# Kernel tuning notes

Hardware: AMD Instinct MI355X
Metric: run time of the kernel (lower is better)

The kernel has to match this reference:

```python
import jax, jax.numpy as jnp
import numpy as np

NEG_SLOPE = 0.2


def gat_layer(h, src, dst, W, al, ar, b, num_nodes):
    # h: [N, Din], W: [Din, H*F], al/ar: [H, F], b: [H*F]
    H, F = al.shape
    feat = (h @ W).reshape(-1, H, F)                      # [N, H, F]
    el = jnp.sum(feat * al[None], axis=-1)                # [N, H]
    er = jnp.sum(feat * ar[None], axis=-1)                # [N, H]
    e = el[src] + er[dst]                                 # [E, H]
    e = jnp.where(e > 0, e, NEG_SLOPE * e)                # leaky_relu(0.2)
    # edge softmax over incoming edges of each dst node (per head)
    m = jax.ops.segment_max(e, dst, num_segments=num_nodes)   # [N, H]
    m = jnp.where(jnp.isfinite(m), m, 0.0)
    a = jnp.exp(e - m[dst])                               # [E, H]
    s = jax.ops.segment_sum(a, dst, num_segments=num_nodes)   # [N, H]
    alpha = a / jnp.maximum(s[dst], 1e-9)                 # [E, H]
    msg = feat[src] * alpha[:, :, None]                   # [E, H, F]
    out = jax.ops.segment_sum(msg, dst, num_segments=num_nodes)  # [N, H, F]
    out = out + b.reshape(H, F)[None]
    return out.reshape(-1, H * F)                         # view(-1, H*F)


def setup_inputs() -> dict:
    key = jax.random.key(0)
    ks = jax.random.split(key, 16)
    N, E, Din, Hh, F = 50000, 800000, 256, 4, 64
    s = 0.05
    return {
        "h": jax.random.normal(ks[0], (N, Din), jnp.float32),
        "src": jax.random.randint(ks[1], (E,), 0, N),
        "dst": jax.random.randint(ks[2], (E,), 0, N),
        "dst_node_ids": jax.random.randint(ks[3], (1024,), 0, N),
        "W0": jax.random.normal(ks[4], (Din, Hh * F), jnp.float32) * s,
        "al0": jax.random.normal(ks[5], (Hh, F), jnp.float32) * s,
        "ar0": jax.random.normal(ks[6], (Hh, F), jnp.float32) * s,
        "b0": jnp.zeros((Hh * F,), jnp.float32),
        "W1": jax.random.normal(ks[7], (Hh * F, Hh * F), jnp.float32) * s,
        "al1": jax.random.normal(ks[8], (Hh, F), jnp.float32) * s,
        "ar1": jax.random.normal(ks[9], (Hh, F), jnp.float32) * s,
        "b1": jnp.zeros((Hh * F,), jnp.float32),
        "W2": jax.random.normal(ks[10], (Hh * F, F), jnp.float32) * s,
        "al2": jax.random.normal(ks[11], (1, F), jnp.float32) * s,
        "ar2": jax.random.normal(ks[12], (1, F), jnp.float32) * s,
        "b2": jnp.zeros((F,), jnp.float32),
    }


def reference(h, src, dst, dst_node_ids,
              W0, al0, ar0, b0, W1, al1, ar1, b1, W2, al2, ar2, b2):
    N = h.shape[0]
    h = h.astype(jnp.float32)
    h = gat_layer(h, src, dst, W0, al0, ar0, b0, N)
    h = gat_layer(h, src, dst, W1, al1, ar1, b1, N)
    h = gat_layer(h, src, dst, W2, al2, ar2, b2, N)
    return h, dst_node_ids
```

## Files before the change

kernel.cpp:

```cpp
#include <hip/hip_runtime.h>
#include <hip/hip_bf16.h>

#define NEG_SLOPE 0.2f

typedef __attribute__((ext_vector_type(8))) short bf16x8;
typedef __attribute__((ext_vector_type(4))) float f32x4;

static inline int cdiv(int a, int b) { return (a + b - 1) / b; }

__device__ inline unsigned short f2bf(float x) {
  __hip_bfloat16 b = __float2bfloat16(x);
  return *reinterpret_cast<unsigned short*>(&b);
}
__device__ inline float bf2f(unsigned short u) {
  unsigned int v = (unsigned int)u << 16;
  return *reinterpret_cast<float*>(&v);
}

__global__ void splitT_all(const float* __restrict__ W0, unsigned short* __restrict__ W0hi,
                           unsigned short* __restrict__ W0lo,
                           const float* __restrict__ W1, unsigned short* __restrict__ W1hi,
                           unsigned short* __restrict__ W1lo,
                           const float* __restrict__ W2, unsigned short* __restrict__ W2hi,
                           unsigned short* __restrict__ W2lo) {
  const int S0 = 256 * 256, S1 = 256 * 256, S2 = 256 * 64;
  int i = blockIdx.x * blockDim.x + threadIdx.x;
  const float* W; unsigned short *hi, *lo; int K, Mo, perm;
  if (i < S0) { W = W0; hi = W0hi; lo = W0lo; K = 256; Mo = 256; perm = 0; }
  else if (i < S0 + S1) { i -= S0; W = W1; hi = W1hi; lo = W1lo; K = 256; Mo = 256; perm = 1; }
  else if (i < S0 + S1 + S2) { i -= S0 + S1; W = W2; hi = W2hi; lo = W2lo; K = 256; Mo = 64; perm = 1; }
  else return;
  int k = i / Mo, m = i - k * Mo;
  int kk = perm ? ((k & 63) * 4 + (k >> 6)) : k;
  float v = W[i];
  unsigned short h = f2bf(v);
  hi[(size_t)m * K + kk] = h;
  lo[(size_t)m * K + kk] = f2bf(v - bf2f(h));
}

template <int NF, bool CVT>
__global__ __launch_bounds__(256) void gemm_split(
    const unsigned short* __restrict__ Ahi, const float* __restrict__ Af32,
    const unsigned short* __restrict__ BThi, const unsigned short* __restrict__ BTlo,
    unsigned short* __restrict__ Chi,
    const float* __restrict__ alv, const float* __restrict__ arv,
    float* __restrict__ el, float* __restrict__ er, int Hn, int M, int K, int Ncols) {
  constexpr int BN = NF * 32;
  __shared__ unsigned short As[128][40];
  __shared__ unsigned short Bs[BN][88];
  const int tid = threadIdx.x;
  const int row0 = blockIdx.x * 128;
  const int col0 = blockIdx.y * BN;
  const int wid = tid >> 6, lane = tid & 63;
  const int wm = wid >> 1, wn = wid & 1;
  const int l15 = lane & 15, lg = lane >> 4;
  f32x4 acc[4][NF];
#pragma unroll
  for (int m = 0; m < 4; ++m)
#pragma unroll
    for (int n = 0; n < NF; ++n) acc[m][n] = (f32x4){0.f, 0.f, 0.f, 0.f};

  const uint4 zero4 = {0u, 0u, 0u, 0u};
  for (int k0 = 0; k0 < K; k0 += 32) {
    {
      int r = tid >> 2;
      const int kg = tid & 3;
#pragma unroll
      for (int it = 0; it < 2; ++it, r += 64) {
        const int grow = row0 + r;
        if constexpr (CVT) {
          float4 f0 = make_float4(0.f, 0.f, 0.f, 0.f), f1 = f0;
          if (grow < M) {
            f0 = *reinterpret_cast<const float4*>(&Af32[(size_t)grow * K + k0 + kg * 8]);
            f1 = *reinterpret_cast<const float4*>(&Af32[(size_t)grow * K + k0 + kg * 8 + 4]);
          }
          unsigned short t[8];
          t[0] = f2bf(f0.x); t[1] = f2bf(f0.y); t[2] = f2bf(f0.z); t[3] = f2bf(f0.w);
          t[4] = f2bf(f1.x); t[5] = f2bf(f1.y); t[6] = f2bf(f1.z); t[7] = f2bf(f1.w);
          *reinterpret_cast<uint4*>(&As[r][kg * 8]) = *reinterpret_cast<const uint4*>(t);
        } else {
          uint4 vh = zero4;
          if (grow < M) vh = *reinterpret_cast<const uint4*>(&Ahi[(size_t)grow * K + k0 + kg * 8]);
          *reinterpret_cast<uint4*>(&As[r][kg * 8]) = vh;
        }
      }
    }
    {
      int r = tid >> 2;
      const int kg = tid & 3;
#pragma unroll
      for (int it = 0; it < BN / 64; ++it, r += 64) {
        const int gcol = col0 + r;
        uint4 vh = *reinterpret_cast<const uint4*>(&BThi[(size_t)gcol * K + k0 + kg * 8]);
        uint4 vl = *reinterpret_cast<const uint4*>(&BTlo[(size_t)gcol * K + k0 + kg * 8]);
        *reinterpret_cast<uint4*>(&Bs[r][kg * 8]) = vh;
        *reinterpret_cast<uint4*>(&Bs[r][48 + kg * 8]) = vl;
      }
    }
    __syncthreads();
    bf16x8 ah[4];
#pragma unroll
    for (int m = 0; m < 4; ++m) {
      const int row = wm * 64 + m * 16 + l15;
      ah[m] = *reinterpret_cast<const bf16x8*>(&As[row][lg * 8]);
    }
#pragma unroll
    for (int n = 0; n < NF; ++n) {
      const int col = wn * (NF * 16) + n * 16 + l15;
      bf16x8 bh = *reinterpret_cast<const bf16x8*>(&Bs[col][lg * 8]);
      bf16x8 bl = *reinterpret_cast<const bf16x8*>(&Bs[col][48 + lg * 8]);
#pragma unroll
      for (int m = 0; m < 4; ++m) {
        acc[m][n] = __builtin_amdgcn_mfma_f32_16x16x32_bf16(ah[m], bh, acc[m][n], 0, 0, 0);
        acc[m][n] = __builtin_amdgcn_mfma_f32_16x16x32_bf16(ah[m], bl, acc[m][n], 0, 0, 0);
      }
    }
    __syncthreads();
  }
  const int hw = (col0 + wn * (NF * 16)) >> 6;
  float alw[NF], arw[NF];
#pragma unroll
  for (int n = 0; n < NF; ++n) {
    const int colg = col0 + wn * (NF * 16) + n * 16 + l15;
    alw[n] = alv[colg];
    arw[n] = arv[colg];
  }
  float pel[4][4] = {{0.f}}, per_[4][4] = {{0.f}};
#pragma unroll
  for (int m = 0; m < 4; ++m) {
#pragma unroll
    for (int n = 0; n < NF; ++n) {
      const int col = col0 + wn * (NF * 16) + n * 16 + l15;
#pragma unroll
      for (int j = 0; j < 4; ++j) {
        const int row = row0 + wm * 64 + m * 16 + lg * 4 + j;
        const float v = acc[m][n][j];
        if (row < M) {
          if constexpr (NF == 4) {
            Chi[(size_t)row * 256 + (col & 63) * 4 + (col >> 6)] = f2bf(v);
          } else {
            Chi[(size_t)row * Ncols + col] = f2bf(v);
          }
        }
        pel[m][j] = fmaf(v, alw[n], pel[m][j]);
        per_[m][j] = fmaf(v, arw[n], per_[m][j]);
      }
    }
  }
  float rl[4][4], rr[4][4];
#pragma unroll
  for (int m = 0; m < 4; ++m) {
#pragma unroll
    for (int j = 0; j < 4; ++j) {
      float vl = pel[m][j], vr = per_[m][j];
#pragma unroll
      for (int off = 1; off < 16; off <<= 1) {
        vl += __shfl_xor(vl, off);
        vr += __shfl_xor(vr, off);
      }
      rl[m][j] = vl; rr[m][j] = vr;
    }
  }
  if constexpr (NF == 4) {
    if (l15 == 0) {
#pragma unroll
      for (int m = 0; m < 4; ++m)
#pragma unroll
        for (int j = 0; j < 4; ++j) {
          const int row = row0 + wm * 64 + m * 16 + lg * 4 + j;
          if (row < M) {
            el[(size_t)row * 4 + hw] = rl[m][j];
            er[(size_t)row * 4 + hw] = rr[m][j];
          }
        }
    }
  } else {
    __shared__ float sl[128], sr[128];
    if (wn == 1 && l15 == 0) {
#pragma unroll
      for (int m = 0; m < 4; ++m)
#pragma unroll
        for (int j = 0; j < 4; ++j) {
          const int lr = wm * 64 + m * 16 + lg * 4 + j;
          sl[lr] = rl[m][j]; sr[lr] = rr[m][j];
        }
    }
    __syncthreads();
    if (wn == 0 && l15 == 0) {
#pragma unroll
      for (int m = 0; m < 4; ++m)
#pragma unroll
        for (int j = 0; j < 4; ++j) {
          const int lr = wm * 64 + m * 16 + lg * 4 + j;
          const int row = row0 + lr;
          if (row < M) {
            el[row] = rl[m][j] + sl[lr];
            er[row] = rr[m][j] + sr[lr];
          }
        }
    }
  }
}

__global__ void hist_kernel(const int* __restrict__ dst, int* __restrict__ deg, int E) {
  int i = blockIdx.x * blockDim.x + threadIdx.x;
  if (i < E) atomicAdd(&deg[dst[i]], 1);
}

__global__ void scan1(const int* __restrict__ deg, int* __restrict__ offs,
                      int* __restrict__ bsums, int N) {
  __shared__ int tmp[256];
  const int tid = threadIdx.x;
  const int i = blockIdx.x * 256 + tid;
  int v = (i < N) ? deg[i] : 0;
  tmp[tid] = v;
  __syncthreads();
  for (int d = 1; d < 256; d <<= 1) {
    int t = (tid >= d) ? tmp[tid - d] : 0;
    __syncthreads();
    tmp[tid] += t;
    __syncthreads();
  }
  if (i < N) offs[i] = tmp[tid] - v;
  if (tid == 255) bsums[blockIdx.x] = tmp[255];
}

__global__ void scan2(int* __restrict__ bsums, int nb) {
  __shared__ int tmp[256];
  const int tid = threadIdx.x;
  int v = (tid < nb) ? bsums[tid] : 0;
  tmp[tid] = v;
  __syncthreads();
  for (int d = 1; d < 256; d <<= 1) {
    int t = (tid >= d) ? tmp[tid - d] : 0;
    __syncthreads();
    tmp[tid] += t;
    __syncthreads();
  }
  if (tid < nb) bsums[tid] = tmp[tid] - v;
}

__global__ void scan3(int* __restrict__ offs, const int* __restrict__ bsums,
                      int* __restrict__ cursor, int N, int E) {
  const int i = blockIdx.x * 256 + threadIdx.x;
  if (i < N) {
    const int v = offs[i] + bsums[blockIdx.x];
    offs[i] = v;
    cursor[i] = v;
  }
  if (i == 0) offs[N] = E;
}

__global__ void scatter_kernel(const int* __restrict__ src, const int* __restrict__ dst,
                               int* __restrict__ cursor, int* __restrict__ csr_src, int E) {
  int i = blockIdx.x * blockDim.x + threadIdx.x;
  if (i >= E) return;
  int pos = atomicAdd(&cursor[dst[i]], 1);
  csr_src[pos] = src[i];
}

template <int H>
__global__ void alpha16(const int* __restrict__ offs, const int* __restrict__ csr_src,
                        const float* __restrict__ el, const float* __restrict__ er,
                        unsigned short* __restrict__ abuf, int N) {
  const int w = (int)((blockIdx.x * (size_t)blockDim.x + threadIdx.x) >> 6);
  const int lane = threadIdx.x & 63;
  const int g = lane >> 4, q = lane & 15;
  const int node = w * 4 + g;
  int beg = 0, end = 0;
  float erh[H];
#pragma unroll
  for (int h = 0; h < H; ++h) erh[h] = 0.f;
  if (node < N) {
    beg = offs[node]; end = offs[node + 1];
    if constexpr (H == 4) {
      float4 t = *reinterpret_cast<const float4*>(&er[(size_t)node * 4]);
      erh[0] = t.x; erh[1] = t.y; erh[2] = t.z; erh[3] = t.w;
    } else {
      erh[0] = er[node];
    }
  }
  float m[H], s[H];
#pragma unroll
  for (int h = 0; h < H; ++h) { m[h] = -INFINITY; s[h] = 0.f; }
  for (int i0 = beg; i0 < end; i0 += 16) {
    const int i = i0 + q;
    const bool valid = i < end;
    const int sn = valid ? csr_src[i] : 0;
    float e[H];
    if constexpr (H == 4) {
      float4 v = *reinterpret_cast<const float4*>(&el[(size_t)sn * 4]);
      e[0] = v.x + erh[0]; e[1] = v.y + erh[1]; e[2] = v.z + erh[2]; e[3] = v.w + erh[3];
    } else {
      e[0] = el[sn] + erh[0];
    }
#pragma unroll
    for (int h = 0; h < H; ++h) {
      e[h] = e[h] > 0.f ? e[h] : NEG_SLOPE * e[h];
      if (!valid) e[h] = -INFINITY;
      float cm = e[h];
#pragma unroll
      for (int off = 1; off < 16; off <<= 1) cm = fmaxf(cm, __shfl_xor(cm, off));
      const float nm = fmaxf(m[h], cm);
      float cs = __expf(e[h] - nm);
#pragma unroll
      for (int off = 1; off < 16; off <<= 1) cs += __shfl_xor(cs, off);
      s[h] = s[h] * __expf(m[h] - nm) + cs;
      m[h] = nm;
    }
  }
  float inv[H];
#pragma unroll
  for (int h = 0; h < H; ++h) inv[h] = 1.f / fmaxf(s[h], 1e-9f);
  for (int i0 = beg; i0 < end; i0 += 16) {
    const int i = i0 + q;
    if (i < end) {
      const int sn = csr_src[i];
      float e[H];
      if constexpr (H == 4) {
        float4 v = *reinterpret_cast<const float4*>(&el[(size_t)sn * 4]);
        e[0] = v.x + erh[0]; e[1] = v.y + erh[1]; e[2] = v.z + erh[2]; e[3] = v.w + erh[3];
      } else {
        e[0] = el[sn] + erh[0];
      }
#pragma unroll
      for (int h = 0; h < H; ++h) {
        e[h] = e[h] > 0.f ? e[h] : NEG_SLOPE * e[h];
        e[h] = __expf(e[h] - m[h]) * inv[h];
      }
      if constexpr (H == 4) {
        ushort4 o;
        o.x = f2bf(e[0]); o.y = f2bf(e[1]); o.z = f2bf(e[2]); o.w = f2bf(e[3]);
        *reinterpret_cast<ushort4*>(&abuf[(size_t)i * 4]) = o;
      } else {
        abuf[i] = f2bf(e[0]);
      }
    }
  }
}

__global__ void aggregate_h4(const int* __restrict__ offs, const int* __restrict__ csr_src,
                             const ushort4* __restrict__ feat4, const ushort4* __restrict__ abuf4,
                             const float* __restrict__ bias, ushort4* __restrict__ out4, int N) {
  const int node = (int)((blockIdx.x * (size_t)blockDim.x + threadIdx.x) >> 6);
  const int lane = threadIdx.x & 63;
  if (node >= N) return;
  const int beg = offs[node], end = offs[node + 1];
  float a0 = 0.f, a1 = 0.f, a2 = 0.f, a3 = 0.f;
  int i = beg;
  for (; i + 7 < end; i += 8) {
    int sn[8]; ushort4 w[8]; ushort4 uv[8];
#pragma unroll
    for (int u = 0; u < 8; ++u) sn[u] = csr_src[i + u];
#pragma unroll
    for (int u = 0; u < 8; ++u) w[u] = abuf4[i + u];
#pragma unroll
    for (int u = 0; u < 8; ++u) uv[u] = feat4[(size_t)sn[u] * 64 + lane];
#pragma unroll
    for (int u = 0; u < 8; ++u) {
      a0 = fmaf(bf2f(w[u].x), bf2f(uv[u].x), a0);
      a1 = fmaf(bf2f(w[u].y), bf2f(uv[u].y), a1);
      a2 = fmaf(bf2f(w[u].z), bf2f(uv[u].z), a2);
      a3 = fmaf(bf2f(w[u].w), bf2f(uv[u].w), a3);
    }
  }
  for (; i < end; ++i) {
    const int sn = csr_src[i];
    const ushort4 w = abuf4[i];
    const ushort4 uv = feat4[(size_t)sn * 64 + lane];
    a0 = fmaf(bf2f(w.x), bf2f(uv.x), a0);
    a1 = fmaf(bf2f(w.y), bf2f(uv.y), a1);
    a2 = fmaf(bf2f(w.z), bf2f(uv.z), a2);
    a3 = fmaf(bf2f(w.w), bf2f(uv.w), a3);
  }
  const float o0 = a0 + bias[lane];
  const float o1 = a1 + bias[64 + lane];
  const float o2 = a2 + bias[128 + lane];
  const float o3 = a3 + bias[192 + lane];
  ushort4 ov;
  ov.x = f2bf(o0); ov.y = f2bf(o1); ov.z = f2bf(o2); ov.w = f2bf(o3);
  out4[(size_t)node * 64 + lane] = ov;
}

__global__ void aggregate1(const int* __restrict__ offs, const int* __restrict__ csr_src,
                           const unsigned short* __restrict__ featH, const unsigned short* __restrict__ abuf,
                           const float* __restrict__ bias, float* __restrict__ outf, int N) {
  const int wid = (int)((blockIdx.x * (size_t)blockDim.x + threadIdx.x) >> 6);
  const int lane = threadIdx.x & 63;
  if (wid >= N) return;
  const int beg = offs[wid], end = offs[wid + 1];
  const int g = lane >> 4, q = lane & 15;
  float4 acc = make_float4(0.f, 0.f, 0.f, 0.f);
  for (int i0 = beg; i0 < end; i0 += 4) {
    const int e = i0 + g;
    if (e < end) {
      const int sn = csr_src[e];
      const float a = bf2f(abuf[e]);
      const ushort4 u = *reinterpret_cast<const ushort4*>(&featH[(size_t)sn * 64 + q * 4]);
      acc.x = fmaf(a, bf2f(u.x), acc.x);
      acc.y = fmaf(a, bf2f(u.y), acc.y);
      acc.z = fmaf(a, bf2f(u.z), acc.z);
      acc.w = fmaf(a, bf2f(u.w), acc.w);
    }
  }
#pragma unroll
  for (int off = 16; off <= 32; off <<= 1) {
    acc.x += __shfl_xor(acc.x, off);
    acc.y += __shfl_xor(acc.y, off);
    acc.z += __shfl_xor(acc.z, off);
    acc.w += __shfl_xor(acc.w, off);
  }
  if (lane < 16) {
    const float4 b4 = *reinterpret_cast<const float4*>(&bias[q * 4]);
    float4 o = make_float4(acc.x + b4.x, acc.y + b4.y, acc.z + b4.z, acc.w + b4.w);
    *reinterpret_cast<float4*>(&outf[(size_t)wid * 64 + q * 4]) = o;
  }
}

__global__ void copy_ids(const int* __restrict__ ids, float* __restrict__ out, int n) {
  int i = blockIdx.x * blockDim.x + threadIdx.x;
  if (i < n) out[i] = (float)ids[i];
}

extern "C" void kernel_launch(void* const* d_in, const int* in_sizes, int n_in,
                              void* d_out, int out_size, void* d_ws, size_t ws_size,
                              hipStream_t stream) {
  const float* h   = (const float*)d_in[0];
  const int* src   = (const int*)d_in[1];
  const int* dst   = (const int*)d_in[2];
  const int* ids   = (const int*)d_in[3];
  const float* W0  = (const float*)d_in[4];
  const float* al0 = (const float*)d_in[5];
  const float* ar0 = (const float*)d_in[6];
  const float* b0  = (const float*)d_in[7];
  const float* W1  = (const float*)d_in[8];
  const float* al1 = (const float*)d_in[9];
  const float* ar1 = (const float*)d_in[10];
  const float* b1  = (const float*)d_in[11];
  const float* W2  = (const float*)d_in[12];
  const float* al2 = (const float*)d_in[13];
  const float* ar2 = (const float*)d_in[14];
  const float* b2  = (const float*)d_in[15];

  const int Din = 256, HF = 256, F2 = 64;
  const int N = in_sizes[0] / Din;
  const int E = in_sizes[1];
  const int NIDS = in_sizes[3];

  char* p = (char*)d_ws;
  unsigned short* Chi = (unsigned short*)p; p += (size_t)N * 256 * 2;
  unsigned short* Ahi = (unsigned short*)p; p += (size_t)N * 256 * 2;
  unsigned short* W0hi = (unsigned short*)p; p += (size_t)HF * Din * 2;
  unsigned short* W0lo = (unsigned short*)p; p += (size_t)HF * Din * 2;
  unsigned short* W1hi = (unsigned short*)p; p += (size_t)HF * HF * 2;
  unsigned short* W1lo = (unsigned short*)p; p += (size_t)HF * HF * 2;
  unsigned short* W2hi = (unsigned short*)p; p += (size_t)F2 * HF * 2;
  unsigned short* W2lo = (unsigned short*)p; p += (size_t)F2 * HF * 2;
  float* el   = (float*)p;             p += (size_t)N * 4 * 4;
  float* er   = (float*)p;             p += (size_t)N * 4 * 4;
  unsigned short* abuf = (unsigned short*)p; p += (size_t)E * 4 * 2;
  int* deg    = (int*)p;               p += (size_t)N * 4;
  int* offs   = (int*)p;               p += (size_t)(N + 16) * 4;
  int* bsums  = (int*)p;               p += 256 * 4;
  int* csr_src = (int*)p;              p += (size_t)E * 4;

  float* outp = (float*)d_out;
  dim3 blk(256);
  const int nb = cdiv(N, 256);
  const int nwAlpha = cdiv(cdiv(N, 4) * 64, 256);

  splitT_all<<<cdiv(256 * 256 * 2 + 256 * 64, 256), blk, 0, stream>>>(
      W0, W0hi, W0lo, W1, W1hi, W1lo, W2, W2hi, W2lo);

  hipMemsetAsync(deg, 0, (size_t)N * 4, stream);
  hist_kernel<<<cdiv(E, 256), blk, 0, stream>>>(dst, deg, E);
  scan1<<<nb, blk, 0, stream>>>(deg, offs, bsums, N);
  scan2<<<1, blk, 0, stream>>>(bsums, nb);
  scan3<<<nb, blk, 0, stream>>>(offs, bsums, deg, N, E);
  scatter_kernel<<<cdiv(E, 256), blk, 0, stream>>>(src, dst, deg, csr_src, E);

  {
    dim3 g(cdiv(N, 128), HF / 128);
    gemm_split<4, true><<<g, blk, 0, stream>>>(nullptr, h, W0hi, W0lo, Chi, al0, ar0, el, er, 4, N, Din, HF);
    alpha16<4><<<nwAlpha, blk, 0, stream>>>(offs, csr_src, el, er, abuf, N);
    aggregate_h4<<<cdiv(N * 64, 256), blk, 0, stream>>>(offs, csr_src, (const ushort4*)Chi,
                                                        (const ushort4*)abuf, b0, (ushort4*)Ahi, N);
  }
  {
    dim3 g(cdiv(N, 128), HF / 128);
    gemm_split<4, false><<<g, blk, 0, stream>>>(Ahi, nullptr, W1hi, W1lo, Chi, al1, ar1, el, er, 4, N, HF, HF);
    alpha16<4><<<nwAlpha, blk, 0, stream>>>(offs, csr_src, el, er, abuf, N);
    aggregate_h4<<<cdiv(N * 64, 256), blk, 0, stream>>>(offs, csr_src, (const ushort4*)Chi,
                                                        (const ushort4*)abuf, b1, (ushort4*)Ahi, N);
  }
  {
    dim3 g(cdiv(N, 128), 1);
    gemm_split<2, false><<<g, blk, 0, stream>>>(Ahi, nullptr, W2hi, W2lo, Chi, al2, ar2, el, er, 1, N, HF, F2);
    alpha16<1><<<nwAlpha, blk, 0, stream>>>(offs, csr_src, el, er, abuf, N);
    aggregate1<<<cdiv(N * 64, 256), blk, 0, stream>>>(offs, csr_src, Chi, abuf, b2, outp, N);
  }
  copy_ids<<<cdiv(NIDS, 256), blk, 0, stream>>>(ids, outp + (size_t)N * F2, NIDS);
}
```

Measured before the change: 401.4 us.

## Drop bf16 lo-split weights and fuse edge softmax into 4-head aggregation

```diff
diff --git a/kernel.cpp b/kernel.cpp
--- a/kernel.cpp
+++ b/kernel.cpp
@@ -18,36 +18,30 @@
 }
 
 __global__ void splitT_all(const float* __restrict__ W0, unsigned short* __restrict__ W0hi,
-                           unsigned short* __restrict__ W0lo,
                            const float* __restrict__ W1, unsigned short* __restrict__ W1hi,
-                           unsigned short* __restrict__ W1lo,
-                           const float* __restrict__ W2, unsigned short* __restrict__ W2hi,
-                           unsigned short* __restrict__ W2lo) {
+                           const float* __restrict__ W2, unsigned short* __restrict__ W2hi) {
   const int S0 = 256 * 256, S1 = 256 * 256, S2 = 256 * 64;
   int i = blockIdx.x * blockDim.x + threadIdx.x;
-  const float* W; unsigned short *hi, *lo; int K, Mo, perm;
-  if (i < S0) { W = W0; hi = W0hi; lo = W0lo; K = 256; Mo = 256; perm = 0; }
-  else if (i < S0 + S1) { i -= S0; W = W1; hi = W1hi; lo = W1lo; K = 256; Mo = 256; perm = 1; }
-  else if (i < S0 + S1 + S2) { i -= S0 + S1; W = W2; hi = W2hi; lo = W2lo; K = 256; Mo = 64; perm = 1; }
+  const float* W; unsigned short* hi; int K, Mo, perm;
+  if (i < S0) { W = W0; hi = W0hi; K = 256; Mo = 256; perm = 0; }
+  else if (i < S0 + S1) { i -= S0; W = W1; hi = W1hi; K = 256; Mo = 256; perm = 1; }
+  else if (i < S0 + S1 + S2) { i -= S0 + S1; W = W2; hi = W2hi; K = 256; Mo = 64; perm = 1; }
   else return;
   int k = i / Mo, m = i - k * Mo;
   int kk = perm ? ((k & 63) * 4 + (k >> 6)) : k;
-  float v = W[i];
-  unsigned short h = f2bf(v);
-  hi[(size_t)m * K + kk] = h;
-  lo[(size_t)m * K + kk] = f2bf(v - bf2f(h));
+  hi[(size_t)m * K + kk] = f2bf(W[i]);
 }
 
 template <int NF, bool CVT>
 __global__ __launch_bounds__(256) void gemm_split(
     const unsigned short* __restrict__ Ahi, const float* __restrict__ Af32,
-    const unsigned short* __restrict__ BThi, const unsigned short* __restrict__ BTlo,
+    const unsigned short* __restrict__ BThi,
     unsigned short* __restrict__ Chi,
     const float* __restrict__ alv, const float* __restrict__ arv,
     float* __restrict__ el, float* __restrict__ er, int Hn, int M, int K, int Ncols) {
   constexpr int BN = NF * 32;
   __shared__ unsigned short As[128][40];
-  __shared__ unsigned short Bs[BN][88];
+  __shared__ unsigned short Bs[BN][40];
   const int tid = threadIdx.x;
   const int row0 = blockIdx.x * 128;
   const int col0 = blockIdx.y * BN;
@@ -92,9 +86,7 @@
       for (int it = 0; it < BN / 64; ++it, r += 64) {
         const int gcol = col0 + r;
         uint4 vh = *reinterpret_cast<const uint4*>(&BThi[(size_t)gcol * K + k0 + kg * 8]);
-        uint4 vl = *reinterpret_cast<const uint4*>(&BTlo[(size_t)gcol * K + k0 + kg * 8]);
         *reinterpret_cast<uint4*>(&Bs[r][kg * 8]) = vh;
-        *reinterpret_cast<uint4*>(&Bs[r][48 + kg * 8]) = vl;
       }
     }
     __syncthreads();
@@ -108,12 +100,9 @@
     for (int n = 0; n < NF; ++n) {
       const int col = wn * (NF * 16) + n * 16 + l15;
       bf16x8 bh = *reinterpret_cast<const bf16x8*>(&Bs[col][lg * 8]);
-      bf16x8 bl = *reinterpret_cast<const bf16x8*>(&Bs[col][48 + lg * 8]);
-#pragma unroll
-      for (int m = 0; m < 4; ++m) {
+#pragma unroll
+      for (int m = 0; m < 4; ++m)
         acc[m][n] = __builtin_amdgcn_mfma_f32_16x16x32_bf16(ah[m], bh, acc[m][n], 0, 0, 0);
-        acc[m][n] = __builtin_amdgcn_mfma_f32_16x16x32_bf16(ah[m], bl, acc[m][n], 0, 0, 0);
-      }
     }
     __syncthreads();
   }
@@ -259,119 +248,109 @@
   csr_src[pos] = src[i];
 }
 
-template <int H>
-__global__ void alpha16(const int* __restrict__ offs, const int* __restrict__ csr_src,
-                        const float* __restrict__ el, const float* __restrict__ er,
-                        unsigned short* __restrict__ abuf, int N) {
-  const int w = (int)((blockIdx.x * (size_t)blockDim.x + threadIdx.x) >> 6);
-  const int lane = threadIdx.x & 63;
-  const int g = lane >> 4, q = lane & 15;
-  const int node = w * 4 + g;
-  int beg = 0, end = 0;
-  float erh[H];
-#pragma unroll
-  for (int h = 0; h < H; ++h) erh[h] = 0.f;
-  if (node < N) {
-    beg = offs[node]; end = offs[node + 1];
-    if constexpr (H == 4) {
-      float4 t = *reinterpret_cast<const float4*>(&er[(size_t)node * 4]);
-      erh[0] = t.x; erh[1] = t.y; erh[2] = t.z; erh[3] = t.w;
-    } else {
-      erh[0] = er[node];
-    }
-  }
-  float m[H], s[H];
-#pragma unroll
-  for (int h = 0; h < H; ++h) { m[h] = -INFINITY; s[h] = 0.f; }
-  for (int i0 = beg; i0 < end; i0 += 16) {
-    const int i = i0 + q;
-    const bool valid = i < end;
-    const int sn = valid ? csr_src[i] : 0;
-    float e[H];
-    if constexpr (H == 4) {
-      float4 v = *reinterpret_cast<const float4*>(&el[(size_t)sn * 4]);
-      e[0] = v.x + erh[0]; e[1] = v.y + erh[1]; e[2] = v.z + erh[2]; e[3] = v.w + erh[3];
-    } else {
-      e[0] = el[sn] + erh[0];
-    }
-#pragma unroll
-    for (int h = 0; h < H; ++h) {
-      e[h] = e[h] > 0.f ? e[h] : NEG_SLOPE * e[h];
-      if (!valid) e[h] = -INFINITY;
-      float cm = e[h];
-#pragma unroll
-      for (int off = 1; off < 16; off <<= 1) cm = fmaxf(cm, __shfl_xor(cm, off));
-      const float nm = fmaxf(m[h], cm);
-      float cs = __expf(e[h] - nm);
-#pragma unroll
-      for (int off = 1; off < 16; off <<= 1) cs += __shfl_xor(cs, off);
-      s[h] = s[h] * __expf(m[h] - nm) + cs;
-      m[h] = nm;
-    }
-  }
-  float inv[H];
-#pragma unroll
-  for (int h = 0; h < H; ++h) inv[h] = 1.f / fmaxf(s[h], 1e-9f);
-  for (int i0 = beg; i0 < end; i0 += 16) {
-    const int i = i0 + q;
-    if (i < end) {
-      const int sn = csr_src[i];
-      float e[H];
-      if constexpr (H == 4) {
-        float4 v = *reinterpret_cast<const float4*>(&el[(size_t)sn * 4]);
-        e[0] = v.x + erh[0]; e[1] = v.y + erh[1]; e[2] = v.z + erh[2]; e[3] = v.w + erh[3];
-      } else {
-        e[0] = el[sn] + erh[0];
-      }
-#pragma unroll
-      for (int h = 0; h < H; ++h) {
-        e[h] = e[h] > 0.f ? e[h] : NEG_SLOPE * e[h];
-        e[h] = __expf(e[h] - m[h]) * inv[h];
-      }
-      if constexpr (H == 4) {
-        ushort4 o;
-        o.x = f2bf(e[0]); o.y = f2bf(e[1]); o.z = f2bf(e[2]); o.w = f2bf(e[3]);
-        *reinterpret_cast<ushort4*>(&abuf[(size_t)i * 4]) = o;
-      } else {
-        abuf[i] = f2bf(e[0]);
-      }
-    }
-  }
-}
-
-__global__ void aggregate_h4(const int* __restrict__ offs, const int* __restrict__ csr_src,
-                             const ushort4* __restrict__ feat4, const ushort4* __restrict__ abuf4,
-                             const float* __restrict__ bias, ushort4* __restrict__ out4, int N) {
+#define CAP 128
+__global__ void agg_fused_h4(const int* __restrict__ offs, const int* __restrict__ csr_src,
+                             const ushort4* __restrict__ feat4, const float* __restrict__ el,
+                             const float* __restrict__ er, const float* __restrict__ bias,
+                             ushort4* __restrict__ out4, int N) {
+  __shared__ float ea[4][CAP][4];
+  const int wslot = threadIdx.x >> 6;
   const int node = (int)((blockIdx.x * (size_t)blockDim.x + threadIdx.x) >> 6);
   const int lane = threadIdx.x & 63;
   if (node >= N) return;
   const int beg = offs[node], end = offs[node + 1];
+  const int deg = end - beg;
+  const float4 erv = *reinterpret_cast<const float4*>(&er[(size_t)node * 4]);
+  float m0 = -INFINITY, m1 = -INFINITY, m2 = -INFINITY, m3 = -INFINITY;
+  float s0 = 0.f, s1 = 0.f, s2 = 0.f, s3 = 0.f;
+  for (int i0 = beg; i0 < end; i0 += 64) {
+    const int i = i0 + lane;
+    const bool valid = i < end;
+    const int sn = valid ? csr_src[i] : 0;
+    const float4 elv = *reinterpret_cast<const float4*>(&el[(size_t)sn * 4]);
+    float e0 = elv.x + erv.x, e1 = elv.y + erv.y, e2 = elv.z + erv.z, e3 = elv.w + erv.w;
+    e0 = e0 > 0.f ? e0 : NEG_SLOPE * e0;
+    e1 = e1 > 0.f ? e1 : NEG_SLOPE * e1;
+    e2 = e2 > 0.f ? e2 : NEG_SLOPE * e2;
+    e3 = e3 > 0.f ? e3 : NEG_SLOPE * e3;
+    if (!valid) { e0 = e1 = e2 = e3 = -INFINITY; }
+    const int sidx = i0 - beg + lane;
+    if (valid && sidx < CAP) {
+      float4 ev; ev.x = e0; ev.y = e1; ev.z = e2; ev.w = e3;
+      *reinterpret_cast<float4*>(&ea[wslot][sidx][0]) = ev;
+    }
+    float cm, cs, nm;
+#define RED(eh, mh, sh)                                                  \
+    cm = eh;                                                             \
+    _Pragma("unroll")                                                    \
+    for (int off = 1; off < 64; off <<= 1) cm = fmaxf(cm, __shfl_xor(cm, off)); \
+    nm = fmaxf(mh, cm);                                                  \
+    cs = __expf(eh - nm);                                                \
+    _Pragma("unroll")                                                    \
+    for (int off = 1; off < 64; off <<= 1) cs += __shfl_xor(cs, off);    \
+    sh = sh * __expf(mh - nm) + cs;                                      \
+    mh = nm;
+    RED(e0, m0, s0) RED(e1, m1, s1) RED(e2, m2, s2) RED(e3, m3, s3)
+#undef RED
+  }
+  const float i0v = 1.f / fmaxf(s0, 1e-9f);
+  const float i1v = 1.f / fmaxf(s1, 1e-9f);
+  const float i2v = 1.f / fmaxf(s2, 1e-9f);
+  const float i3v = 1.f / fmaxf(s3, 1e-9f);
+  const int cap = deg < CAP ? deg : CAP;
+  for (int sidx = lane; sidx < cap; sidx += 64) {
+    float4 ev = *reinterpret_cast<const float4*>(&ea[wslot][sidx][0]);
+    float4 av;
+    av.x = __expf(ev.x - m0) * i0v;
+    av.y = __expf(ev.y - m1) * i1v;
+    av.z = __expf(ev.z - m2) * i2v;
+    av.w = __expf(ev.w - m3) * i3v;
+    *reinterpret_cast<float4*>(&ea[wslot][sidx][0]) = av;
+  }
+  auto alphaOf = [&](int sn) -> float4 {
+    const float4 elv = *reinterpret_cast<const float4*>(&el[(size_t)sn * 4]);
+    float e0x = elv.x + erv.x, e1x = elv.y + erv.y, e2x = elv.z + erv.z, e3x = elv.w + erv.w;
+    e0x = e0x > 0.f ? e0x : NEG_SLOPE * e0x;
+    e1x = e1x > 0.f ? e1x : NEG_SLOPE * e1x;
+    e2x = e2x > 0.f ? e2x : NEG_SLOPE * e2x;
+    e3x = e3x > 0.f ? e3x : NEG_SLOPE * e3x;
+    float4 r;
+    r.x = __expf(e0x - m0) * i0v; r.y = __expf(e1x - m1) * i1v;
+    r.z = __expf(e2x - m2) * i2v; r.w = __expf(e3x - m3) * i3v;
+    return r;
+  };
   float a0 = 0.f, a1 = 0.f, a2 = 0.f, a3 = 0.f;
   int i = beg;
   for (; i + 7 < end; i += 8) {
-    int sn[8]; ushort4 w[8]; ushort4 uv[8];
+    int sn[8]; float4 aw[8]; ushort4 uv[8];
 #pragma unroll
     for (int u = 0; u < 8; ++u) sn[u] = csr_src[i + u];
 #pragma unroll
-    for (int u = 0; u < 8; ++u) w[u] = abuf4[i + u];
+    for (int u = 0; u < 8; ++u) {
+      const int sidx = i + u - beg;
+      aw[u] = (sidx < CAP) ? *reinterpret_cast<const float4*>(&ea[wslot][sidx][0])
+                           : alphaOf(sn[u]);
+    }
 #pragma unroll
     for (int u = 0; u < 8; ++u) uv[u] = feat4[(size_t)sn[u] * 64 + lane];
 #pragma unroll
     for (int u = 0; u < 8; ++u) {
-      a0 = fmaf(bf2f(w[u].x), bf2f(uv[u].x), a0);
-      a1 = fmaf(bf2f(w[u].y), bf2f(uv[u].y), a1);
-      a2 = fmaf(bf2f(w[u].z), bf2f(uv[u].z), a2);
-      a3 = fmaf(bf2f(w[u].w), bf2f(uv[u].w), a3);
+      a0 = fmaf(aw[u].x, bf2f(uv[u].x), a0);
+      a1 = fmaf(aw[u].y, bf2f(uv[u].y), a1);
+      a2 = fmaf(aw[u].z, bf2f(uv[u].z), a2);
+      a3 = fmaf(aw[u].w, bf2f(uv[u].w), a3);
     }
   }
   for (; i < end; ++i) {
     const int sn = csr_src[i];
-    const ushort4 w = abuf4[i];
+    const int sidx = i - beg;
+    const float4 aw = (sidx < CAP) ? *reinterpret_cast<const float4*>(&ea[wslot][sidx][0])
+                                   : alphaOf(sn);
     const ushort4 uv = feat4[(size_t)sn * 64 + lane];
-    a0 = fmaf(bf2f(w.x), bf2f(uv.x), a0);
-    a1 = fmaf(bf2f(w.y), bf2f(uv.y), a1);
-    a2 = fmaf(bf2f(w.z), bf2f(uv.z), a2);
-    a3 = fmaf(bf2f(w.w), bf2f(uv.w), a3);
+    a0 = fmaf(aw.x, bf2f(uv.x), a0);
+    a1 = fmaf(aw.y, bf2f(uv.y), a1);
+    a2 = fmaf(aw.z, bf2f(uv.z), a2);
+    a3 = fmaf(aw.w, bf2f(uv.w), a3);
   }
   const float o0 = a0 + bias[lane];
   const float o1 = a1 + bias[64 + lane];
@@ -380,6 +359,47 @@
   ushort4 ov;
   ov.x = f2bf(o0); ov.y = f2bf(o1); ov.z = f2bf(o2); ov.w = f2bf(o3);
   out4[(size_t)node * 64 + lane] = ov;
+}
+#undef CAP
+
+__global__ void alpha16_h1(const int* __restrict__ offs, const int* __restrict__ csr_src,
+                           const float* __restrict__ el, const float* __restrict__ er,
+                           unsigned short* __restrict__ abuf, int N) {
+  const int w = (int)((blockIdx.x * (size_t)blockDim.x + threadIdx.x) >> 6);
+  const int lane = threadIdx.x & 63;
+  const int g = lane >> 4, q = lane & 15;
+  const int node = w * 4 + g;
+  int beg = 0, end = 0;
+  float erh = 0.f;
+  if (node < N) { beg = offs[node]; end = offs[node + 1]; erh = er[node]; }
+  float m = -INFINITY, s = 0.f;
+  for (int i0 = beg; i0 < end; i0 += 16) {
+    const int i = i0 + q;
+    const bool valid = i < end;
+    const int sn = valid ? csr_src[i] : 0;
+    float e = el[sn] + erh;
+    e = e > 0.f ? e : NEG_SLOPE * e;
+    if (!valid) e = -INFINITY;
+    float cm = e;
+#pragma unroll
+    for (int off = 1; off < 16; off <<= 1) cm = fmaxf(cm, __shfl_xor(cm, off));
+    const float nm = fmaxf(m, cm);
+    float cs = __expf(e - nm);
+#pragma unroll
+    for (int off = 1; off < 16; off <<= 1) cs += __shfl_xor(cs, off);
+    s = s * __expf(m - nm) + cs;
+    m = nm;
+  }
+  const float inv = 1.f / fmaxf(s, 1e-9f);
+  for (int i0 = beg; i0 < end; i0 += 16) {
+    const int i = i0 + q;
+    if (i < end) {
+      const int sn = csr_src[i];
+      float e = el[sn] + erh;
+      e = e > 0.f ? e : NEG_SLOPE * e;
+      abuf[i] = f2bf(__expf(e - m) * inv);
+    }
+  }
 }
 
 __global__ void aggregate1(const int* __restrict__ offs, const int* __restrict__ csr_src,
@@ -451,14 +471,11 @@
   unsigned short* Chi = (unsigned short*)p; p += (size_t)N * 256 * 2;
   unsigned short* Ahi = (unsigned short*)p; p += (size_t)N * 256 * 2;
   unsigned short* W0hi = (unsigned short*)p; p += (size_t)HF * Din * 2;
-  unsigned short* W0lo = (unsigned short*)p; p += (size_t)HF * Din * 2;
   unsigned short* W1hi = (unsigned short*)p; p += (size_t)HF * HF * 2;
-  unsigned short* W1lo = (unsigned short*)p; p += (size_t)HF * HF * 2;
   unsigned short* W2hi = (unsigned short*)p; p += (size_t)F2 * HF * 2;
-  unsigned short* W2lo = (unsigned short*)p; p += (size_t)F2 * HF * 2;
   float* el   = (float*)p;             p += (size_t)N * 4 * 4;
   float* er   = (float*)p;             p += (size_t)N * 4 * 4;
-  unsigned short* abuf = (unsigned short*)p; p += (size_t)E * 4 * 2;
+  unsigned short* abuf = (unsigned short*)p; p += (size_t)E * 2;
   int* deg    = (int*)p;               p += (size_t)N * 4;
   int* offs   = (int*)p;               p += (size_t)(N + 16) * 4;
   int* bsums  = (int*)p;               p += 256 * 4;
@@ -467,10 +484,9 @@
   float* outp = (float*)d_out;
   dim3 blk(256);
   const int nb = cdiv(N, 256);
-  const int nwAlpha = cdiv(cdiv(N, 4) * 64, 256);
 
   splitT_all<<<cdiv(256 * 256 * 2 + 256 * 64, 256), blk, 0, stream>>>(
-      W0, W0hi, W0lo, W1, W1hi, W1lo, W2, W2hi, W2lo);
+      W0, W0hi, W1, W1hi, W2, W2hi);
 
   hipMemsetAsync(deg, 0, (size_t)N * 4, stream);
   hist_kernel<<<cdiv(E, 256), blk, 0, stream>>>(dst, deg, E);
@@ -481,22 +497,20 @@
 
   {
     dim3 g(cdiv(N, 128), HF / 128);
-    gemm_split<4, true><<<g, blk, 0, stream>>>(nullptr, h, W0hi, W0lo, Chi, al0, ar0, el, er, 4, N, Din, HF);
-    alpha16<4><<<nwAlpha, blk, 0, stream>>>(offs, csr_src, el, er, abuf, N);
-    aggregate_h4<<<cdiv(N * 64, 256), blk, 0, stream>>>(offs, csr_src, (const ushort4*)Chi,
-                                                        (const ushort4*)abuf, b0, (ushort4*)Ahi, N);
+    gemm_split<4, true><<<g, blk, 0, stream>>>(nullptr, h, W0hi, Chi, al0, ar0, el, er, 4, N, Din, HF);
+    agg_fused_h4<<<cdiv(N * 64, 256), blk, 0, stream>>>(offs, csr_src, (const ushort4*)Chi,
+                                                        el, er, b0, (ushort4*)Ahi, N);
   }
   {
     dim3 g(cdiv(N, 128), HF / 128);
-    gemm_split<4, false><<<g, blk, 0, stream>>>(Ahi, nullptr, W1hi, W1lo, Chi, al1, ar1, el, er, 4, N, HF, HF);
-    alpha16<4><<<nwAlpha, blk, 0, stream>>>(offs, csr_src, el, er, abuf, N);
-    aggregate_h4<<<cdiv(N * 64, 256), blk, 0, stream>>>(offs, csr_src, (const ushort4*)Chi,
-                                                        (const ushort4*)abuf, b1, (ushort4*)Ahi, N);
+    gemm_split<4, false><<<g, blk, 0, stream>>>(Ahi, nullptr, W1hi, Chi, al1, ar1, el, er, 4, N, HF, HF);
+    agg_fused_h4<<<cdiv(N * 64, 256), blk, 0, stream>>>(offs, csr_src, (const ushort4*)Chi,
+                                                        el, er, b1, (ushort4*)Ahi, N);
   }
   {
     dim3 g(cdiv(N, 128), 1);
-    gemm_split<2, false><<<g, blk, 0, stream>>>(Ahi, nullptr, W2hi, W2lo, Chi, al2, ar2, el, er, 1, N, HF, F2);
-    alpha16<1><<<nwAlpha, blk, 0, stream>>>(offs, csr_src, el, er, abuf, N);
+    gemm_split<2, false><<<g, blk, 0, stream>>>(Ahi, nullptr, W2hi, Chi, al2, ar2, el, er, 1, N, HF, F2);
+    alpha16_h1<<<cdiv(cdiv(N, 4) * 64, 256), blk, 0, stream>>>(offs, csr_src, el, er, abuf, N);
     aggregate1<<<cdiv(N * 64, 256), blk, 0, stream>>>(offs, csr_src, Chi, abuf, b2, outp, N);
   }
   copy_ids<<<cdiv(NIDS, 256), blk, 0, stream>>>(ids, outp + (size_t)N * F2, NIDS);
```

After: 439.6 us. 1.1x slower.
